# Optimization experiments

Hardware: AMD Instinct MI355X
Metric: run time of the kernel (lower is better)

Reference implementation:

```python
import jax, jax.numpy as jnp
import numpy as np

EPS = 1e-5  # BatchNorm1d default eps
N1, N2 = 4096, 4096


def _encoder(x, W1, b1, W2, b2, W3, b3, gamma, beta):
    # fc1: Linear(node_num,256)+ReLU; fc2: Linear(256,128)+ReLU; fc3: Linear(128,64)+BN(train-mode)+ReLU
    h = jax.nn.relu(x @ W1.T + b1)
    h = jax.nn.relu(h @ W2.T + b2)
    h = h @ W3.T + b3
    m = h.mean(axis=0)
    v = ((h - m) ** 2).mean(axis=0)  # biased variance, as BN training mode
    return jax.nn.relu((h - m) / jnp.sqrt(v + EPS) * gamma + beta)


def _self_attention(x, adj, alpha):
    # vectorized form of the per-node double loop:
    # tmp_i = (sum_{j: adj[i,j]==1} alpha[i,j] * x[j]) / degree_i + x[i]  if degree_i != 0 else 0
    mask = (adj == 1.0).astype(x.dtype)           # [N,N]
    deg = adj.sum(axis=1, keepdims=True)          # [N,1]
    agg = (mask * alpha) @ x                      # [N,64] masked SpMM
    return jnp.where(deg != 0, agg / deg + x, jnp.zeros((), x.dtype))


def setup_inputs() -> dict:
    key = jax.random.key(0)
    ks = jax.random.split(key, 20)
    d = {}
    d["x1"] = jax.random.normal(ks[0], (N1, N1), jnp.float32)
    d["x2"] = jax.random.normal(ks[1], (N2, N2), jnp.float32)
    d["adj1"] = jax.random.bernoulli(ks[2], 0.01, (N1, N1)).astype(jnp.float32)
    d["adj2"] = jax.random.bernoulli(ks[3], 0.01, (N2, N2)).astype(jnp.float32)
    def lin(k, fan_out, fan_in):
        bound = 1.0 / np.sqrt(fan_in)
        k1, k2 = jax.random.split(k)
        return (jax.random.uniform(k1, (fan_out, fan_in), jnp.float32, -bound, bound),
                jax.random.uniform(k2, (fan_out,), jnp.float32, -bound, bound))
    d["e1_W1"], d["e1_b1"] = lin(ks[4], 256, N1)
    d["e1_W2"], d["e1_b2"] = lin(ks[5], 128, 256)
    d["e1_W3"], d["e1_b3"] = lin(ks[6], 64, 128)
    d["e1_gamma"] = jnp.ones((64,), jnp.float32)
    d["e1_beta"] = jnp.zeros((64,), jnp.float32)
    d["e2_W1"], d["e2_b1"] = lin(ks[7], 256, N2)
    d["e2_W2"], d["e2_b2"] = lin(ks[8], 128, 256)
    d["e2_W3"], d["e2_b3"] = lin(ks[9], 64, 128)
    d["e2_gamma"] = jnp.ones((64,), jnp.float32)
    d["e2_beta"] = jnp.zeros((64,), jnp.float32)
    d["alpha1"] = jax.random.uniform(ks[10], (N1, N1), jnp.float32)
    d["alpha2"] = jax.random.uniform(ks[11], (N2, N2), jnp.float32)
    d["Wc"], d["bc"] = lin(ks[12], 2, (N1 + N2) * 64)
    return d


def reference(x1, x2, adj1, adj2,
              e1_W1, e1_b1, e1_W2, e1_b2, e1_W3, e1_b3, e1_gamma, e1_beta,
              e2_W1, e2_b1, e2_W2, e2_b2, e2_W3, e2_b3, e2_gamma, e2_beta,
              alpha1, alpha2, Wc, bc):
    h1 = _encoder(x1, e1_W1, e1_b1, e1_W2, e1_b2, e1_W3, e1_b3, e1_gamma, e1_beta)
    h2 = _encoder(x2, e2_W1, e2_b1, e2_W2, e2_b2, e2_W3, e2_b3, e2_gamma, e2_beta)
    h1 = _self_attention(h1, adj1, alpha1)
    h2 = _self_attention(h2, adj2, alpha2)
    feat = jnp.concatenate([h1, h2], axis=0).reshape(1, -1)  # [1,(N1+N2)*64]
    return feat @ Wc.T + bc  # [1,2] logits (softmax is defined but unused in forward)
```

## Files before the change

### kernel.cpp

```cpp
#include <hip/hip_runtime.h>
#include <cstddef>
#include <cstdint>


#define NN 4096
#define HDIM 64
#define ENC_OUT (NN * HDIM)

typedef _Float16 half8 __attribute__((ext_vector_type(8)));
typedef _Float16 half4 __attribute__((ext_vector_type(4)));
typedef float v4f __attribute__((ext_vector_type(4)));

__device__ __forceinline__ void gld_lds16(const void* g, void* l) {
    __builtin_amdgcn_global_load_lds(
        (const __attribute__((address_space(1))) void*)g,
        (__attribute__((address_space(3))) void*)l, 16, 0, 0);
}

struct GemmP {
    const void*     A[2];
    const _Float16* B[2];
    const float*    bias[2];
    void*           C[2];
};

__global__ __launch_bounds__(1024, 4) void fc1_kernel(GemmP p)
{
    __shared__ char lds[64 * 1024];

    const int tid = threadIdx.x;
    const int wave = tid >> 6, lane = tid & 63;
    const int l16 = lane & 15, quad = lane >> 4;
    const int kg = wave >> 2, ng = wave & 3;
    const int enc = blockIdx.y;
    const int m0 = blockIdx.x * 32;
    const int kOff = kg * 1024;
    constexpr int NS = 32;

    const float* __restrict__ A = (const float*)p.A[enc];
    const _Float16* __restrict__ Bp = p.B[enc];

    const int srow = ng * 8 + (lane >> 3);
    const int schunk = (lane & 7) ^ ((lane >> 3) & 7);
    const float* asrc0 = A + (size_t)(m0 + srow) * NN + kOff + schunk * 4;
    char* f32base = &lds[kg * 8192 + ng * 1024];
    char* f16kg   = &lds[32768 + kg * 4096];

    const int f16woff = (schunk >> 1) * 512 + srow * 16 + (schunk & 1) * 8;

    const int frag0 = quad * 512 + l16 * 16;
    const int frag1 = quad * 512 + (16 + l16) * 16;

    const _Float16* bsrc = Bp + (size_t)(ng * 64 + l16) * NN + kOff + quad * 8;

    v4f acc[2][4];
#pragma unroll
    for (int mi = 0; mi < 2; mi++)
#pragma unroll
        for (int ni = 0; ni < 4; ni++) acc[mi][ni] = (v4f){0.f, 0.f, 0.f, 0.f};

    half8 b0[4], b1[4];

    gld_lds16(asrc0, f32base);
#pragma unroll
    for (int ni = 0; ni < 4; ni++)
        b0[ni] = *(const half8*)(bsrc + (size_t)ni * 16 * NN);
    gld_lds16(asrc0 + 32, f32base + 4096);
    __builtin_amdgcn_sched_barrier(0);
    __builtin_amdgcn_s_waitcnt(0x0F75);
    __builtin_amdgcn_sched_barrier(0);
    {
        float4 f = *(const float4*)(f32base + lane * 16);
        half4 h;
        h[0] = (_Float16)f.x; h[1] = (_Float16)f.y;
        h[2] = (_Float16)f.z; h[3] = (_Float16)f.w;
        *(half4*)(f16kg + f16woff) = h;
    }
    __builtin_amdgcn_sched_barrier(0);
    __builtin_amdgcn_s_waitcnt(0x3F7F & 0xC07F);
    __builtin_amdgcn_sched_barrier(0);
    __builtin_amdgcn_s_barrier();

    auto body = [&](int s, half8* bcur, half8* bnxt) {
        if (s + 1 < NS) {
#pragma unroll
            for (int ni = 0; ni < 4; ni++)
                bnxt[ni] = *(const half8*)(bsrc + (size_t)ni * 16 * NN + (s + 1) * 32);
        }
        if (s + 2 < NS)
            gld_lds16(asrc0 + (s + 2) * 32, f32base + ((s + 2) & 1) * 4096);
        __builtin_amdgcn_sched_barrier(0);
        if (s + 2 < NS)      __builtin_amdgcn_s_waitcnt(0x0F75);
        else if (s + 1 < NS) __builtin_amdgcn_s_waitcnt(0x0F74);
        else                 __builtin_amdgcn_s_waitcnt(0x0F70);
        __builtin_amdgcn_sched_barrier(0);
        if (s + 1 < NS) {
            float4 f = *(const float4*)(f32base + ((s + 1) & 1) * 4096 + lane * 16);
            half4 h;
            h[0] = (_Float16)f.x; h[1] = (_Float16)f.y;
            h[2] = (_Float16)f.z; h[3] = (_Float16)f.w;
            *(half4*)(f16kg + ((s + 1) & 1) * 2048 + f16woff) = h;
        }
        const char* fb = f16kg + (s & 1) * 2048;
        half8 ca0 = *(const half8*)(fb + frag0);
        half8 ca1 = *(const half8*)(fb + frag1);
#pragma unroll
        for (int ni = 0; ni < 4; ni++) {
            acc[0][ni] = __builtin_amdgcn_mfma_f32_16x16x32_f16(ca0, bcur[ni], acc[0][ni], 0, 0, 0);
            acc[1][ni] = __builtin_amdgcn_mfma_f32_16x16x32_f16(ca1, bcur[ni], acc[1][ni], 0, 0, 0);
        }
        __builtin_amdgcn_sched_barrier(0);
        __builtin_amdgcn_s_waitcnt(0xC07F);
        __builtin_amdgcn_sched_barrier(0);
        __builtin_amdgcn_s_barrier();
    };

    for (int s = 0; s < NS; s += 2) {
        body(s, b0, b1);
        body(s + 1, b1, b0);
    }

    __syncthreads();

    if (kg >= 2) {
        const int sidx = (kg - 2) * 4 + ng;
#pragma unroll
        for (int mi = 0; mi < 2; mi++)
#pragma unroll
            for (int ni = 0; ni < 4; ni++)
                *(v4f*)&lds[sidx * 8192 + (mi * 4 + ni) * 1024 + lane * 16] = acc[mi][ni];
    }
    __syncthreads();
    if (kg < 2) {
        const int sidx = kg * 4 + ng;
#pragma unroll
        for (int mi = 0; mi < 2; mi++)
#pragma unroll
            for (int ni = 0; ni < 4; ni++)
                acc[mi][ni] += *(const v4f*)&lds[sidx * 8192 + (mi * 4 + ni) * 1024 + lane * 16];
    }
    __syncthreads();

    if (kg == 1) {
#pragma unroll
        for (int mi = 0; mi < 2; mi++)
#pragma unroll
            for (int ni = 0; ni < 4; ni++)
                *(v4f*)&lds[ng * 8192 + (mi * 4 + ni) * 1024 + lane * 16] = acc[mi][ni];
    }
    __syncthreads();

    if (kg == 0) {
        _Float16* __restrict__ h1 = (_Float16*)p.C[enc];
        const float* __restrict__ bs = p.bias[enc];
#pragma unroll
        for (int mi = 0; mi < 2; mi++)
#pragma unroll
            for (int ni = 0; ni < 4; ni++) {
                v4f v = acc[mi][ni] + *(const v4f*)&lds[ng * 8192 + (mi * 4 + ni) * 1024 + lane * 16];
                const int col = ng * 64 + ni * 16 + l16;
                const float b = bs[col];
#pragma unroll
                for (int i = 0; i < 4; i++) {
                    const int row = m0 + mi * 16 + quad * 4 + i;
                    h1[(size_t)row * 256 + col] = (_Float16)fmaxf(v[i] + b, 0.f);
                }
            }
    }
}

template<int NI, bool A16, int OUT, bool RELU>
__global__ __launch_bounds__(256) void gemm_kernel(GemmP p, int M, int lda, int Ksub)
{
    constexpr int N = NI * 64;
    __shared__ char Bs[NI * 4 * 1024];

    const int tid = threadIdx.x;
    const int wave = tid >> 6, lane = tid & 63;
    const int l16 = lane & 15, quad = lane >> 4;
    const int enc = blockIdx.z, split = blockIdx.x;
    const int m0 = blockIdx.y * 32;
    const int kOff = split * Ksub;
    const int nsteps = Ksub >> 5;

    const _Float16* __restrict__ Bp = p.B[enc];
    const char* Abase = (const char*)p.A[enc];

    const size_t aoff0 = (size_t)(m0 + l16) * lda + kOff + quad * 8;
    const size_t aoff1 = aoff0 + (size_t)16 * lda;

    half8 na0, na1;
    float4 nf0lo, nf0hi, nf1lo, nf1hi;
    auto loadA = [&](int s) {
        if constexpr (A16) {
            const _Float16* A = (const _Float16*)Abase;
            na0 = *(const half8*)(A + aoff0 + s * 32);
            na1 = *(const half8*)(A + aoff1 + s * 32);
        } else {
            const float* A = (const float*)Abase;
            nf0lo = *(const float4*)(A + aoff0 + s * 32);
            nf0hi = *(const float4*)(A + aoff0 + s * 32 + 4);
            nf1lo = *(const float4*)(A + aoff1 + s * 32);
            nf1hi = *(const float4*)(A + aoff1 + s * 32 + 4);
        }
    };

    v4f acc[2][NI];
#pragma unroll
    for (int mi = 0; mi < 2; mi++)
#pragma unroll
        for (int ni = 0; ni < NI; ni++) acc[mi][ni] = (v4f){0.f, 0.f, 0.f, 0.f};

    loadA(0);

    for (int s = 0; s < nsteps; ++s) {
#pragma unroll
        for (int ni = 0; ni < NI; ni++) {
            const int T = wave * NI + ni;
            const _Float16* g = Bp + (size_t)(T * 16 + l16) * lda + kOff + s * 32 + quad * 8;
            gld_lds16(g, &Bs[T * 1024]);
        }
        half8 ca0, ca1;
        if constexpr (A16) {
            ca0 = na0; ca1 = na1;
        } else {
            ca0[0] = (_Float16)nf0lo.x; ca0[1] = (_Float16)nf0lo.y;
            ca0[2] = (_Float16)nf0lo.z; ca0[3] = (_Float16)nf0lo.w;
            ca0[4] = (_Float16)nf0hi.x; ca0[5] = (_Float16)nf0hi.y;
            ca0[6] = (_Float16)nf0hi.z; ca0[7] = (_Float16)nf0hi.w;
            ca1[0] = (_Float16)nf1lo.x; ca1[1] = (_Float16)nf1lo.y;
            ca1[2] = (_Float16)nf1lo.z; ca1[3] = (_Float16)nf1lo.w;
            ca1[4] = (_Float16)nf1hi.x; ca1[5] = (_Float16)nf1hi.y;
            ca1[6] = (_Float16)nf1hi.z; ca1[7] = (_Float16)nf1hi.w;
        }
        if (s + 1 < nsteps) loadA(s + 1);

        __builtin_amdgcn_s_waitcnt(0x0F70);

#pragma unroll
        for (int ni = 0; ni < NI; ni++) {
            half8 bf = *(const half8*)&Bs[(wave * NI + ni) * 1024 + lane * 16];
            acc[0][ni] = __builtin_amdgcn_mfma_f32_16x16x32_f16(ca0, bf, acc[0][ni], 0, 0, 0);
            acc[1][ni] = __builtin_amdgcn_mfma_f32_16x16x32_f16(ca1, bf, acc[1][ni], 0, 0, 0);
        }
    }

#pragma unroll
    for (int mi = 0; mi < 2; mi++)
#pragma unroll
        for (int ni = 0; ni < NI; ni++) {
            const int col = wave * NI * 16 + ni * 16 + l16;
#pragma unroll
            for (int i = 0; i < 4; i++) {
                const int row = m0 + mi * 16 + quad * 4 + i;
                float v = acc[mi][ni][i];
                v += p.bias[enc][col];
                if (RELU) v = fmaxf(v, 0.f);
                if constexpr (OUT == 0)
                    ((_Float16*)p.C[enc])[(size_t)row * N + col] = (_Float16)v;
                else
                    ((float*)p.C[enc])[(size_t)row * N + col] = v;
            }
        }
}

struct CvtJob { const float* s; _Float16* d; int n4; };
struct CvtP { CvtJob j[6]; };

__global__ __launch_bounds__(256) void cvt_all_kernel(CvtP p)
{
    int i = blockIdx.x * 256 + threadIdx.x;
#pragma unroll
    for (int k = 0; k < 6; k++) {
        if (i < p.j[k].n4) {
            float4 v = ((const float4*)p.j[k].s)[i];
            half4 h;
            h[0] = (_Float16)v.x; h[1] = (_Float16)v.y;
            h[2] = (_Float16)v.z; h[3] = (_Float16)v.w;
            ((half4*)p.j[k].d)[i] = h;
            return;
        }
        i -= p.j[k].n4;
    }
}

__global__ __launch_bounds__(256) void bn_stat1_kernel(const float* __restrict__ h3,
                                                       float* __restrict__ bnp)
{
    const int enc = blockIdx.y, b = blockIdx.x;
    const int c = threadIdx.x & 63, rg = threadIdx.x >> 6;
    const float* h = h3 + (size_t)enc * ENC_OUT + (size_t)b * 128 * HDIM;
    float s = 0.f, q = 0.f;
    for (int r = rg; r < 128; r += 4) {
        float v = h[(size_t)r * HDIM + c];
        s += v; q += v * v;
    }
    __shared__ float ss[4][64], sq[4][64];
    ss[rg][c] = s; sq[rg][c] = q;
    __syncthreads();
    if (threadIdx.x < 64) {
        float S = ss[0][c] + ss[1][c] + ss[2][c] + ss[3][c];
        float Q = sq[0][c] + sq[1][c] + sq[2][c] + sq[3][c];
        bnp[(size_t)(enc * 32 + b) * 128 + c] = S;
        bnp[(size_t)(enc * 32 + b) * 128 + 64 + c] = Q;
    }
}

__global__ void bn_stat2_kernel(const float* __restrict__ bnp, float* __restrict__ stats)
{
    const int enc = blockIdx.x, c = threadIdx.x;
    float s = 0.f, q = 0.f;
    for (int b = 0; b < 32; b++) {
        s += bnp[(size_t)(enc * 32 + b) * 128 + c];
        q += bnp[(size_t)(enc * 32 + b) * 128 + 64 + c];
    }
    float mean = s * (1.f / NN);
    float var = q * (1.f / NN) - mean * mean;
    stats[enc * 128 + c] = mean;
    stats[enc * 128 + 64 + c] = rsqrtf(var + 1e-5f);
}

__global__ __launch_bounds__(256) void bn_apply_kernel(const float* __restrict__ h3,
                                                       const float* __restrict__ stats,
                                                       const float* __restrict__ g0,
                                                       const float* __restrict__ g1,
                                                       const float* __restrict__ be0,
                                                       const float* __restrict__ be1,
                                                       float* __restrict__ hn)
{
    const int idx = blockIdx.x * 256 + threadIdx.x;
    const int enc = idx >> 18;
    const int c = idx & 63;
    const float* g = enc ? g1 : g0;
    const float* be = enc ? be1 : be0;
    const float m = stats[enc * 128 + c];
    const float rs = stats[enc * 128 + 64 + c];
    float v = (h3[idx] - m) * rs * g[c] + be[c];
    hn[idx] = fmaxf(v, 0.f);
}

__global__ __launch_bounds__(256) void att_kernel(const float* __restrict__ adj1,
                                                  const float* __restrict__ adj2,
                                                  const float* __restrict__ al1,
                                                  const float* __restrict__ al2,
                                                  const float* __restrict__ hn,
                                                  float* __restrict__ out)
{
    const int enc = blockIdx.y;
    const float* adj = enc ? adj2 : adj1;
    const float* al = enc ? al2 : al1;
    const float* h = hn + (size_t)enc * ENC_OUT;
    float* o = out + (size_t)enc * ENC_OUT;
    const int i = blockIdx.x;
    const int tid = threadIdx.x;

    __shared__ int s_cnt;
    __shared__ int s_j[128];
    __shared__ float s_w[128];
    __shared__ float s_acc[4][64];

    if (tid == 0) s_cnt = 0;
    __syncthreads();

    const float* arow = adj + (size_t)i * NN;
    const int jb = tid * 16;
#pragma unroll
    for (int q = 0; q < 4; q++) {
        float4 a = *(const float4*)&arow[jb + q * 4];
        if (a.x == 1.f) { int p = atomicAdd(&s_cnt, 1); if (p < 128) s_j[p] = jb + q * 4 + 0; }
        if (a.y == 1.f) { int p = atomicAdd(&s_cnt, 1); if (p < 128) s_j[p] = jb + q * 4 + 1; }
        if (a.z == 1.f) { int p = atomicAdd(&s_cnt, 1); if (p < 128) s_j[p] = jb + q * 4 + 2; }
        if (a.w == 1.f) { int p = atomicAdd(&s_cnt, 1); if (p < 128) s_j[p] = jb + q * 4 + 3; }
    }
    __syncthreads();
    const int cnt = min(s_cnt, 128);

    const float* alrow = al + (size_t)i * NN;
    for (int t = tid; t < cnt; t += 256) s_w[t] = alrow[s_j[t]];
    __syncthreads();

    const int c = tid & 63;
    const int g = tid >> 6;
    float acc = 0.f;
    for (int t = g; t < cnt; t += 4) acc += s_w[t] * h[(size_t)s_j[t] * HDIM + c];
    s_acc[g][c] = acc;
    __syncthreads();

    if (tid < 64) {
        float r;
        if (cnt != 0) {
            r = (s_acc[0][c] + s_acc[1][c] + s_acc[2][c] + s_acc[3][c]) / (float)cnt
                + h[(size_t)i * HDIM + c];
        } else {
            r = 0.f;
        }
        o[(size_t)i * HDIM + c] = r;
    }
}

#define FDIM (2 * ENC_OUT)

__global__ __launch_bounds__(256) void final_partial_kernel(const float* __restrict__ feat,
                                                            const float* __restrict__ Wc,
                                                            float* __restrict__ partial)
{
    const int gt = blockIdx.x * 256 + threadIdx.x;
    float p0 = 0.f, p1 = 0.f;
    for (int f = gt; f < FDIM; f += 131072) {
        float x = feat[f];
        p0 += x * Wc[f];
        p1 += x * Wc[FDIM + f];
    }
    __shared__ float r0[256], r1[256];
    r0[threadIdx.x] = p0;
    r1[threadIdx.x] = p1;
    __syncthreads();
    for (int off = 128; off > 0; off >>= 1) {
        if (threadIdx.x < off) {
            r0[threadIdx.x] += r0[threadIdx.x + off];
            r1[threadIdx.x] += r1[threadIdx.x + off];
        }
        __syncthreads();
    }
    if (threadIdx.x == 0) {
        partial[blockIdx.x * 2 + 0] = r0[0];
        partial[blockIdx.x * 2 + 1] = r1[0];
    }
}

__global__ __launch_bounds__(256) void final_reduce_kernel(const float* __restrict__ partial,
                                                           const float* __restrict__ bc,
                                                           float* __restrict__ out)
{
    const int t = threadIdx.x;
    float2 v = ((const float2*)partial)[t];
    float2 w = ((const float2*)partial)[t + 256];
    __shared__ float r0[256], r1[256];
    r0[t] = v.x + w.x;
    r1[t] = v.y + w.y;
    __syncthreads();
    for (int off = 128; off > 0; off >>= 1) {
        if (t < off) {
            r0[t] += r0[t + off];
            r1[t] += r1[t + off];
        }
        __syncthreads();
    }
    if (t == 0) {
        out[0] = bc[0] + r0[0];
        out[1] = bc[1] + r1[0];
    }
}


extern "C" void kernel_launch(void* const* d_in, const int* in_sizes, int n_in,
                              void* d_out, int out_size, void* d_ws, size_t ws_size,
                              hipStream_t stream)
{
    const float* x1    = (const float*)d_in[0];
    const float* x2    = (const float*)d_in[1];
    const float* adj1  = (const float*)d_in[2];
    const float* adj2  = (const float*)d_in[3];
    const float* e1_W1 = (const float*)d_in[4];
    const float* e1_b1 = (const float*)d_in[5];
    const float* e1_W2 = (const float*)d_in[6];
    const float* e1_b2 = (const float*)d_in[7];
    const float* e1_W3 = (const float*)d_in[8];
    const float* e1_b3 = (const float*)d_in[9];
    const float* e1_g  = (const float*)d_in[10];
    const float* e1_be = (const float*)d_in[11];
    const float* e2_W1 = (const float*)d_in[12];
    const float* e2_b1 = (const float*)d_in[13];
    const float* e2_W2 = (const float*)d_in[14];
    const float* e2_b2 = (const float*)d_in[15];
    const float* e2_W3 = (const float*)d_in[16];
    const float* e2_b3 = (const float*)d_in[17];
    const float* e2_g  = (const float*)d_in[18];
    const float* e2_be = (const float*)d_in[19];
    const float* alpha1 = (const float*)d_in[20];
    const float* alpha2 = (const float*)d_in[21];
    const float* Wc    = (const float*)d_in[22];
    const float* bc    = (const float*)d_in[23];
    (void)in_sizes; (void)n_in; (void)out_size; (void)ws_size;

    char* w = (char*)d_ws;
    _Float16* W1h = (_Float16*)w;  w += (size_t)2 * 256 * NN * 2;
    _Float16* W2h = (_Float16*)w;  w += (size_t)2 * 128 * 256 * 2;
    _Float16* W3h = (_Float16*)w;  w += (size_t)2 * 64 * 128 * 2;
    _Float16* h1h = (_Float16*)w;  w += (size_t)2 * NN * 256 * 2;
    char* shared8 = w;             w += (size_t)8 * 1024 * 1024;
    float* bnp = (float*)w;        w += (size_t)2 * 32 * 128 * 4;
    float* stats = (float*)w;      w += 256 * 4;
    float* hpart = (float*)w;      w += 1024 * 4;

    _Float16* h2h  = (_Float16*)shared8;
    float* h3  = (float*)(shared8 + 2 * 1024 * 1024);
    float* hn  = (float*)(shared8 + 4 * 1024 * 1024);
    float* att = (float*)(shared8 + 6 * 1024 * 1024);

    const dim3 blk(256);

    CvtP cp;
    cp.j[0] = { e1_W1, W1h,             262144 };
    cp.j[1] = { e2_W1, W1h + 256 * NN,  262144 };
    cp.j[2] = { e1_W2, W2h,             8192 };
    cp.j[3] = { e2_W2, W2h + 128 * 256, 8192 };
    cp.j[4] = { e1_W3, W3h,             2048 };
    cp.j[5] = { e2_W3, W3h + 64 * 128,  2048 };
    cvt_all_kernel<<<dim3(2128), blk, 0, stream>>>(cp);

    GemmP p1 = { {x1, x2}, {W1h, W1h + 256 * NN}, {e1_b1, e2_b1},
                 {h1h, h1h + (size_t)NN * 256} };
    fc1_kernel<<<dim3(NN / 32, 2), dim3(1024), 0, stream>>>(p1);

    GemmP p2 = { {h1h, h1h + (size_t)NN * 256}, {W2h, W2h + 128 * 256}, {e1_b2, e2_b2},
                 {h2h, h2h + (size_t)NN * 128} };
    gemm_kernel<2, true, 0, true><<<dim3(1, NN / 32, 2), blk, 0, stream>>>(p2, NN, 256, 256);

    GemmP p3 = { {h2h, h2h + (size_t)NN * 128}, {W3h, W3h + 64 * 128}, {e1_b3, e2_b3},
                 {h3, h3 + ENC_OUT} };
    gemm_kernel<1, true, 1, false><<<dim3(1, NN / 32, 2), blk, 0, stream>>>(p3, NN, 128, 128);

    bn_stat1_kernel<<<dim3(32, 2), blk, 0, stream>>>(h3, bnp);
    bn_stat2_kernel<<<dim3(2), dim3(64), 0, stream>>>(bnp, stats);
    bn_apply_kernel<<<dim3(2 * ENC_OUT / 256), blk, 0, stream>>>(h3, stats, e1_g, e2_g,
                                                                 e1_be, e2_be, hn);

    att_kernel<<<dim3(NN, 2), blk, 0, stream>>>(adj1, adj2, alpha1, alpha2, hn, att);

    final_partial_kernel<<<dim3(512), blk, 0, stream>>>(att, Wc, hpart);
    final_reduce_kernel<<<dim3(1), blk, 0, stream>>>(hpart, bc, (float*)d_out);
}
```

Measured before the change: 469.8 us.

## Restructure fc1 pipeline to register-staged A, ballot-based attention compaction

```diff
diff --git a/kernel.cpp b/kernel.cpp
--- a/kernel.cpp
+++ b/kernel.cpp
@@ -24,7 +24,7 @@
     void*           C[2];
 };
 
-__global__ __launch_bounds__(1024, 4) void fc1_kernel(GemmP p)
+__global__ __launch_bounds__(1024) void fc1_kernel(GemmP p)
 {
     __shared__ char lds[64 * 1024];
 
@@ -35,21 +35,21 @@
     const int enc = blockIdx.y;
     const int m0 = blockIdx.x * 32;
     const int kOff = kg * 1024;
-    constexpr int NS = 32;
+    constexpr int NS = 16;
 
     const float* __restrict__ A = (const float*)p.A[enc];
     const _Float16* __restrict__ Bp = p.B[enc];
 
     const int srow = ng * 8 + (lane >> 3);
-    const int schunk = (lane & 7) ^ ((lane >> 3) & 7);
-    const float* asrc0 = A + (size_t)(m0 + srow) * NN + kOff + schunk * 4;
-    char* f32base = &lds[kg * 8192 + ng * 1024];
-    char* f16kg   = &lds[32768 + kg * 4096];
-
-    const int f16woff = (schunk >> 1) * 512 + srow * 16 + (schunk & 1) * 8;
-
-    const int frag0 = quad * 512 + l16 * 16;
-    const int frag1 = quad * 512 + (16 + l16) * 16;
+    const int sc   = lane & 7;
+    const float* asrc = A + (size_t)(m0 + srow) * NN + kOff + sc * 4;
+
+    char* f16kg = &lds[kg * 8192];
+    const int wof = srow * 64 + (((sc >> 1) ^ ((srow >> 1) & 3)) * 16) + (sc & 1) * 8;
+
+    const int r0 = l16, r1 = 16 + l16;
+    const int rd0 = r0 * 64 + ((quad ^ ((r0 >> 1) & 3)) * 16);
+    const int rd1 = r1 * 64 + ((quad ^ ((r1 >> 1) & 3)) * 16);
 
     const _Float16* bsrc = Bp + (size_t)(ng * 64 + l16) * NN + kOff + quad * 8;
 
@@ -59,66 +59,54 @@
 #pragma unroll
         for (int ni = 0; ni < 4; ni++) acc[mi][ni] = (v4f){0.f, 0.f, 0.f, 0.f};
 
-    half8 b0[4], b1[4];
-
-    gld_lds16(asrc0, f32base);
-#pragma unroll
-    for (int ni = 0; ni < 4; ni++)
-        b0[ni] = *(const half8*)(bsrc + (size_t)ni * 16 * NN);
-    gld_lds16(asrc0 + 32, f32base + 4096);
-    __builtin_amdgcn_sched_barrier(0);
-    __builtin_amdgcn_s_waitcnt(0x0F75);
-    __builtin_amdgcn_sched_barrier(0);
-    {
-        float4 f = *(const float4*)(f32base + lane * 16);
-        half4 h;
-        h[0] = (_Float16)f.x; h[1] = (_Float16)f.y;
-        h[2] = (_Float16)f.z; h[3] = (_Float16)f.w;
-        *(half4*)(f16kg + f16woff) = h;
-    }
-    __builtin_amdgcn_sched_barrier(0);
-    __builtin_amdgcn_s_waitcnt(0x3F7F & 0xC07F);
-    __builtin_amdgcn_sched_barrier(0);
-    __builtin_amdgcn_s_barrier();
-
-    auto body = [&](int s, half8* bcur, half8* bnxt) {
-        if (s + 1 < NS) {
+    float4 aA[2], aB[2];
+    aA[0] = *(const float4*)(asrc);
+    aA[1] = *(const float4*)(asrc + 32);
+
+    auto body = [&](int s, float4* cur, float4* nxt, bool last) {
+        half8 b[2][4];
+#pragma unroll
+        for (int kq = 0; kq < 2; kq++)
 #pragma unroll
             for (int ni = 0; ni < 4; ni++)
-                bnxt[ni] = *(const half8*)(bsrc + (size_t)ni * 16 * NN + (s + 1) * 32);
-        }
-        if (s + 2 < NS)
-            gld_lds16(asrc0 + (s + 2) * 32, f32base + ((s + 2) & 1) * 4096);
+                b[kq][ni] = *(const half8*)(bsrc + (size_t)ni * 16 * NN + s * 64 + kq * 32);
+        if (!last) {
+            nxt[0] = *(const float4*)(asrc + (s + 1) * 64);
+            nxt[1] = *(const float4*)(asrc + (s + 1) * 64 + 32);
+        }
         __builtin_amdgcn_sched_barrier(0);
-        if (s + 2 < NS)      __builtin_amdgcn_s_waitcnt(0x0F75);
-        else if (s + 1 < NS) __builtin_amdgcn_s_waitcnt(0x0F74);
-        else                 __builtin_amdgcn_s_waitcnt(0x0F70);
-        __builtin_amdgcn_sched_barrier(0);
-        if (s + 1 < NS) {
-            float4 f = *(const float4*)(f32base + ((s + 1) & 1) * 4096 + lane * 16);
+
+        char* fb = f16kg + (s & 1) * 4096;
+#pragma unroll
+        for (int j = 0; j < 2; j++) {
             half4 h;
-            h[0] = (_Float16)f.x; h[1] = (_Float16)f.y;
-            h[2] = (_Float16)f.z; h[3] = (_Float16)f.w;
-            *(half4*)(f16kg + ((s + 1) & 1) * 2048 + f16woff) = h;
-        }
-        const char* fb = f16kg + (s & 1) * 2048;
-        half8 ca0 = *(const half8*)(fb + frag0);
-        half8 ca1 = *(const half8*)(fb + frag1);
-#pragma unroll
-        for (int ni = 0; ni < 4; ni++) {
-            acc[0][ni] = __builtin_amdgcn_mfma_f32_16x16x32_f16(ca0, bcur[ni], acc[0][ni], 0, 0, 0);
-            acc[1][ni] = __builtin_amdgcn_mfma_f32_16x16x32_f16(ca1, bcur[ni], acc[1][ni], 0, 0, 0);
-        }
-        __builtin_amdgcn_sched_barrier(0);
+            h[0] = (_Float16)cur[j].x; h[1] = (_Float16)cur[j].y;
+            h[2] = (_Float16)cur[j].z; h[3] = (_Float16)cur[j].w;
+            *(half4*)(fb + j * 2048 + wof) = h;
+        }
         __builtin_amdgcn_s_waitcnt(0xC07F);
         __builtin_amdgcn_sched_barrier(0);
         __builtin_amdgcn_s_barrier();
+        __builtin_amdgcn_sched_barrier(0);
+        half8 a0k0 = *(const half8*)(fb + rd0);
+        half8 a1k0 = *(const half8*)(fb + rd1);
+        half8 a0k1 = *(const half8*)(fb + 2048 + rd0);
+        half8 a1k1 = *(const half8*)(fb + 2048 + rd1);
+#pragma unroll
+        for (int ni = 0; ni < 4; ni++) {
+            acc[0][ni] = __builtin_amdgcn_mfma_f32_16x16x32_f16(a0k0, b[0][ni], acc[0][ni], 0, 0, 0);
+            acc[0][ni] = __builtin_amdgcn_mfma_f32_16x16x32_f16(a0k1, b[1][ni], acc[0][ni], 0, 0, 0);
+            acc[1][ni] = __builtin_amdgcn_mfma_f32_16x16x32_f16(a1k0, b[0][ni], acc[1][ni], 0, 0, 0);
+            acc[1][ni] = __builtin_amdgcn_mfma_f32_16x16x32_f16(a1k1, b[1][ni], acc[1][ni], 0, 0, 0);
+        }
     };
 
-    for (int s = 0; s < NS; s += 2) {
-        body(s, b0, b1);
-        body(s + 1, b1, b0);
-    }
+    for (int s = 0; s < NS - 2; s += 2) {
+        body(s, aA, aB, false);
+        body(s + 1, aB, aA, false);
+    }
+    body(NS - 2, aA, aB, false);
+    body(NS - 1, aB, aA, true);
 
     __syncthreads();
 
@@ -220,6 +208,7 @@
             const _Float16* g = Bp + (size_t)(T * 16 + l16) * lda + kOff + s * 32 + quad * 8;
             gld_lds16(g, &Bs[T * 1024]);
         }
+        __builtin_amdgcn_sched_barrier(0);
         half8 ca0, ca1;
         if constexpr (A16) {
             ca0 = na0; ca1 = na1;
@@ -233,9 +222,13 @@
             ca1[4] = (_Float16)nf1hi.x; ca1[5] = (_Float16)nf1hi.y;
             ca1[6] = (_Float16)nf1hi.z; ca1[7] = (_Float16)nf1hi.w;
         }
-        if (s + 1 < nsteps) loadA(s + 1);
-
-        __builtin_amdgcn_s_waitcnt(0x0F70);
+        const bool more = (s + 1 < nsteps);
+        if (more) loadA(s + 1);
+        __builtin_amdgcn_sched_barrier(0);
+
+        if (more) __builtin_amdgcn_s_waitcnt(0x0F72);
+        else      __builtin_amdgcn_s_waitcnt(0x0F70);
+        __builtin_amdgcn_sched_barrier(0);
 
 #pragma unroll
         for (int ni = 0; ni < NI; ni++) {
@@ -353,36 +346,52 @@
     float* o = out + (size_t)enc * ENC_OUT;
     const int i = blockIdx.x;
     const int tid = threadIdx.x;
-
-    __shared__ int s_cnt;
-    __shared__ int s_j[128];
-    __shared__ float s_w[128];
+    const int lane = tid & 63;
+    const int w = tid >> 6;
+
+    __shared__ int s_j[192];
+    __shared__ float s_w[192];
+    __shared__ int s_wc[4];
     __shared__ float s_acc[4][64];
 
-    if (tid == 0) s_cnt = 0;
-    __syncthreads();
-
     const float* arow = adj + (size_t)i * NN;
-    const int jb = tid * 16;
-#pragma unroll
-    for (int q = 0; q < 4; q++) {
-        float4 a = *(const float4*)&arow[jb + q * 4];
-        if (a.x == 1.f) { int p = atomicAdd(&s_cnt, 1); if (p < 128) s_j[p] = jb + q * 4 + 0; }
-        if (a.y == 1.f) { int p = atomicAdd(&s_cnt, 1); if (p < 128) s_j[p] = jb + q * 4 + 1; }
-        if (a.z == 1.f) { int p = atomicAdd(&s_cnt, 1); if (p < 128) s_j[p] = jb + q * 4 + 2; }
-        if (a.w == 1.f) { int p = atomicAdd(&s_cnt, 1); if (p < 128) s_j[p] = jb + q * 4 + 3; }
-    }
-    __syncthreads();
-    const int cnt = min(s_cnt, 128);
+
+    unsigned long long masks[16];
+    int cnt_w = 0;
+#pragma unroll
+    for (int r = 0; r < 16; ++r) {
+        float a = arow[w * 1024 + r * 64 + lane];
+        unsigned long long m = __ballot(a == 1.f);
+        masks[r] = m;
+        cnt_w += __popcll(m);
+    }
+    if (lane == 0) s_wc[w] = cnt_w;
+    __syncthreads();
+
+    const int c0 = s_wc[0], c1 = s_wc[1], c2 = s_wc[2], c3 = s_wc[3];
+    const int cnt = c0 + c1 + c2 + c3;
+    const int cc = min(cnt, 192);
+    int run = (w > 0 ? c0 : 0) + (w > 1 ? c1 : 0) + (w > 2 ? c2 : 0);
+
+#pragma unroll
+    for (int r = 0; r < 16; ++r) {
+        unsigned long long m = masks[r];
+        if ((m >> lane) & 1ull) {
+            int pos = run + __popcll(m & ((1ull << lane) - 1ull));
+            if (pos < 192) s_j[pos] = w * 1024 + r * 64 + lane;
+        }
+        run += __popcll(m);
+    }
+    __syncthreads();
 
     const float* alrow = al + (size_t)i * NN;
-    for (int t = tid; t < cnt; t += 256) s_w[t] = alrow[s_j[t]];
+    for (int t = tid; t < cc; t += 256) s_w[t] = alrow[s_j[t]];
     __syncthreads();
 
     const int c = tid & 63;
     const int g = tid >> 6;
     float acc = 0.f;
-    for (int t = g; t < cnt; t += 4) acc += s_w[t] * h[(size_t)s_j[t] * HDIM + c];
+    for (int t = g; t < cc; t += 4) acc += s_w[t] * h[(size_t)s_j[t] * HDIM + c];
     s_acc[g][c] = acc;
     __syncthreads();
 
```

New measurement: 435.0 us. -7.4%, faster.
